# Kernel tuning notes

Measured on AMD Instinct MI355X. Metric: run time of the kernel, lower is better.

The kernel has to match this reference:

```python
import jax, jax.numpy as jnp
import numpy as np

E, QE, P, H = 3, 60000, 40, 20   # elements, atoms per element, fp length, hidden
NIMG = 1800                       # images in batch
Q = E * QE                        # total atoms
NNZ = 14_400_000                  # nnz of sparse fprimes [P*Q, 3*Q]


def setup_inputs() -> dict:
    key = jax.random.key(0)
    ks = jax.random.split(key, 12)
    fps = jax.random.normal(ks[0], (E, QE, P), jnp.float32)
    image_idx = jax.random.randint(ks[1], (E, QE), 0, NIMG, jnp.int32)
    s1 = 1.0 / np.sqrt(P)
    s2 = 1.0 / np.sqrt(H)
    W1 = (jax.random.normal(ks[2], (E, P, H)) * s1).astype(jnp.float32)
    b1 = jnp.zeros((E, H), jnp.float32)
    W2 = (jax.random.normal(ks[3], (E, H, H)) * s2).astype(jnp.float32)
    b2 = jnp.zeros((E, H), jnp.float32)
    W3 = (jax.random.normal(ks[4], (E, H, 1)) * s2).astype(jnp.float32)
    b3 = jnp.zeros((E, 1), jnp.float32)
    fp_rows = jax.random.randint(ks[5], (NNZ,), 0, P * Q, jnp.int32)
    fp_cols = jax.random.randint(ks[6], (NNZ,), 0, 3 * Q, jnp.int32)
    fp_vals = (jax.random.normal(ks[7], (NNZ,)) * 0.05).astype(jnp.float32)
    return {"fps": fps, "W1": W1, "b1": b1, "W2": W2, "b2": b2, "W3": W3,
            "b3": b3, "image_idx": image_idx, "fp_rows": fp_rows,
            "fp_cols": fp_cols, "fp_vals": fp_vals, "batch_size": NIMG}


def _mlp(x, w1, b1, w2, b2, w3, b3):
    # Dense(tanh) -> Dense(tanh) -> Dense(linear), per amptorch MLP(n_layers=3)
    h = jnp.tanh(x @ w1 + b1)
    h = jnp.tanh(h @ w2 + b2)
    return h @ w3 + b3  # [..., 1]


def _esum(x, w1, b1, w2, b2, w3, b3):
    return _mlp(x, w1, b1, w2, b2, w3, b3).sum()


def reference(fps, W1, b1, W2, b2, W3, b3, image_idx, fp_rows, fp_cols,
              fp_vals, batch_size):
    # per-element atomwise energies: [E, QE, 1]
    atom_e = jax.vmap(_mlp)(fps, W1, b1, W2, b2, W3, b3)
    # scatter-add atomic energies into per-image energies (index_add_)
    energy_pred = jax.ops.segment_sum(
        atom_e.reshape(-1, 1), image_idx.reshape(-1).astype(jnp.int32),
        num_segments=batch_size)  # [NIMG, 1]
    # dE/dFP per atom (each atom's output depends only on its own fp, so
    # grad of the per-element energy sum == per-atom jacobian rows)
    dE_dFP = jax.vmap(jax.grad(_esum))(fps, W1, b1, W2, b2, W3, b3)  # [E,QE,P]
    # reorder atoms from element-grouped order to image-index order
    # (stable argsort == boolean-match reorder in the torch code)
    order = jnp.argsort(image_idx.reshape(-1))
    dE_flat = dE_dFP.reshape(-1, P)[order].reshape(-1)  # [P*Q]
    # force = -fprimes^T @ dE_dFP  (sparse COO matvec via segment_sum)
    force_flat = -jax.ops.segment_sum(
        fp_vals * dE_flat[fp_rows], fp_cols, num_segments=3 * Q)
    force_pred = force_flat.reshape(-1, 3)  # [Q, 3]
    return energy_pred, force_pred
```

## Files before the change

kernel.cpp:

```cpp
#include <hip/hip_runtime.h>
#include <math.h>

#define E_    3
#define QE_   60000
#define QTOT  180000
#define P_    40
#define H_    20
#define NIMG_ 1800
#define NNZ_  14400000
#define BLK   256
#define NB    704

#define CW_BITS 12
#define CW      4096
#define NBIN    132
#define SUBS    8
#define SC      8192
#define NSB     1758
#define CAPB    114688

#define C_SCUR  0
#define C_BCUR  64
#define C_INTS  256

typedef int   vi4 __attribute__((ext_vector_type(4)));
typedef float vf4 __attribute__((ext_vector_type(4)));
typedef unsigned uint32;

__global__ void zero_kernel(float* __restrict__ out, int n) {
    int i = blockIdx.x * blockDim.x + threadIdx.x;
    if (i < n) out[i] = 0.0f;
}
__global__ void zero_ctrl_kernel(int* __restrict__ ctrl) {
    ctrl[threadIdx.x] = 0;
}

__global__ void hist_kernel(const int* __restrict__ img, int* __restrict__ g_hist) {
    __shared__ int h[NIMG_];
    const int t = threadIdx.x, b = blockIdx.x;
    for (int v = t; v < NIMG_; v += BLK) h[v] = 0;
    __syncthreads();
    int a = b * BLK + t;
    if (a < QTOT) atomicAdd(&h[img[a]], 1);
    __syncthreads();
    for (int v = t; v < NIMG_; v += BLK) g_hist[v * NB + b] = h[v];
}

__global__ void scan_blocks_kernel(int* __restrict__ g_hist, int* __restrict__ g_total) {
    __shared__ int s[BLK];
    const int v = blockIdx.x, t = threadIdx.x;
    int carry = 0;
    for (int c = 0; c < NB; c += BLK) {
        int idx = c + t;
        int val = (idx < NB) ? g_hist[v * NB + idx] : 0;
        s[t] = val; __syncthreads();
        for (int off = 1; off < BLK; off <<= 1) {
            int tmp = (t >= off) ? s[t - off] : 0;
            __syncthreads();
            s[t] += tmp;
            __syncthreads();
        }
        int excl = s[t] - val;
        int tot  = s[BLK - 1];
        if (idx < NB) g_hist[v * NB + idx] = carry + excl;
        carry += tot;
        __syncthreads();
    }
    if (t == 0) g_total[v] = carry;
}

__global__ void scan_buckets_kernel(const int* __restrict__ g_total, int* __restrict__ g_base) {
    __shared__ int s[BLK];
    const int t = threadIdx.x;
    int carry = 0;
    for (int c = 0; c < NIMG_; c += BLK) {
        int idx = c + t;
        int val = (idx < NIMG_) ? g_total[idx] : 0;
        s[t] = val; __syncthreads();
        for (int off = 1; off < BLK; off <<= 1) {
            int tmp = (t >= off) ? s[t - off] : 0;
            __syncthreads();
            s[t] += tmp;
            __syncthreads();
        }
        if (idx < NIMG_) g_base[idx] = carry + (s[t] - val);
        carry += s[BLK - 1];
        __syncthreads();
    }
}

__global__ void rank_kernel(const int* __restrict__ img, const int* __restrict__ g_hist,
                            const int* __restrict__ g_base, int* __restrict__ rank) {
    __shared__ int simg[BLK];
    const int t = threadIdx.x, b = blockIdx.x;
    int a = b * BLK + t;
    int v = (a < QTOT) ? img[a] : -1;
    simg[t] = v;
    __syncthreads();
    if (a < QTOT) {
        int local = 0;
        for (int j = 0; j < t; ++j) {
            if (simg[j] == v) local++;
        }
        rank[a] = g_base[v] + g_hist[v * NB + b] + local;
    }
}

__global__ __launch_bounds__(BLK) void mlp_kernel(
    const float* __restrict__ fps, const float* __restrict__ W1, const float* __restrict__ b1,
    const float* __restrict__ W2, const float* __restrict__ b2, const float* __restrict__ W3,
    const float* __restrict__ b3, const int* __restrict__ img, const int* __restrict__ rank,
    float* __restrict__ energy, float* __restrict__ dEflat)
{
    __shared__ float sW1[P_ * H_], sW2[H_ * H_], sW3[H_], sB1[H_], sB2[H_];
    __shared__ float sB3;
    const int e = blockIdx.y;
    const int t = threadIdx.x;
    for (int i = t; i < P_ * H_; i += BLK) sW1[i] = W1[e * P_ * H_ + i];
    for (int i = t; i < H_ * H_; i += BLK) sW2[i] = W2[e * H_ * H_ + i];
    if (t < H_) { sW3[t] = W3[e * H_ + t]; sB1[t] = b1[e * H_ + t]; sB2[t] = b2[e * H_ + t]; }
    if (t == 0) sB3 = b3[e];
    __syncthreads();

    int q = blockIdx.x * BLK + t;
    if (q >= QE_) return;
    int a = e * QE_ + q;

    const vf4* xp = (const vf4*)(fps + (size_t)a * P_);
    float x[P_];
    #pragma unroll
    for (int p = 0; p < P_; p += 4) {
        vf4 v4 = __builtin_nontemporal_load(xp + (p >> 2));
        x[p] = v4.x; x[p+1] = v4.y; x[p+2] = v4.z; x[p+3] = v4.w;
    }

    float h1v[H_], h2v[H_];
    #pragma unroll
    for (int i = 0; i < H_; ++i) {
        float z = sB1[i];
        #pragma unroll
        for (int p = 0; p < P_; ++p) z += x[p] * sW1[p * H_ + i];
        h1v[i] = tanhf(z);
    }
    #pragma unroll
    for (int i = 0; i < H_; ++i) {
        float z = sB2[i];
        #pragma unroll
        for (int j = 0; j < H_; ++j) z += h1v[j] * sW2[j * H_ + i];
        h2v[i] = tanhf(z);
    }
    float ea = sB3;
    #pragma unroll
    for (int i = 0; i < H_; ++i) ea += h2v[i] * sW3[i];
    atomicAdd(&energy[img[a]], ea);

    float dz2[H_];
    #pragma unroll
    for (int i = 0; i < H_; ++i) dz2[i] = sW3[i] * (1.0f - h2v[i] * h2v[i]);
    float dz1[H_];
    #pragma unroll
    for (int i = 0; i < H_; ++i) {
        float d = 0.0f;
        #pragma unroll
        for (int j = 0; j < H_; ++j) d += sW2[i * H_ + j] * dz2[j];
        dz1[i] = d * (1.0f - h1v[i] * h1v[i]);
    }
    float* op = dEflat + (size_t)rank[a] * P_;
    #pragma unroll
    for (int p = 0; p < P_; p += 4) {
        float4 v4;
        float d0 = 0.f, d1 = 0.f, d2 = 0.f, d3 = 0.f;
        #pragma unroll
        for (int i = 0; i < H_; ++i) {
            d0 += sW1[(p    ) * H_ + i] * dz1[i];
            d1 += sW1[(p + 1) * H_ + i] * dz1[i];
            d2 += sW1[(p + 2) * H_ + i] * dz1[i];
            d3 += sW1[(p + 3) * H_ + i] * dz1[i];
        }
        v4.x = d0; v4.y = d1; v4.z = d2; v4.w = d3;
        *(float4*)(op + p) = v4;
    }
}

__global__ __launch_bounds__(BLK) void binscatter_kernel(
    const int* __restrict__ rows, const int* __restrict__ cols, const float* __restrict__ vals,
    const float* __restrict__ dEflat, int* __restrict__ ctrl, uint32* __restrict__ bm)
{
    __shared__ uint32 itl[SC];
    __shared__ unsigned char bns[SC];
    __shared__ int hist[NBIN];
    __shared__ int cursor[NBIN];
    __shared__ int delta[NBIN];
    __shared__ int s[BLK];
    const int t = threadIdx.x, b = blockIdx.x;
    const int base = b * SC;
    const int nIt = min(SC, NNZ_ - base);
    const bool full = (nIt == SC);

    if (t < NBIN) hist[t] = 0;
    __syncthreads();
    if (full) {
        const vi4* c4 = (const vi4*)(cols + base);
        #pragma unroll
        for (int j = 0; j < SC / (BLK * 4); ++j) {
            vi4 cc = __builtin_nontemporal_load(c4 + j * BLK + t);
            atomicAdd(&hist[cc.x >> CW_BITS], 1);
            atomicAdd(&hist[cc.y >> CW_BITS], 1);
            atomicAdd(&hist[cc.z >> CW_BITS], 1);
            atomicAdd(&hist[cc.w >> CW_BITS], 1);
        }
    } else {
        for (int j = t; j < nIt; j += BLK)
            atomicAdd(&hist[cols[base + j] >> CW_BITS], 1);
    }
    __syncthreads();
    {
        int v = (t < NBIN) ? hist[t] : 0;
        s[t] = v; __syncthreads();
        for (int off = 1; off < BLK; off <<= 1) {
            int tmp = (t >= off) ? s[t - off] : 0;
            __syncthreads();
            s[t] += tmp;
            __syncthreads();
        }
        if (t < NBIN) {
            int ls = s[t] - v;
            cursor[t] = ls;
            int gb = (v > 0) ? atomicAdd(&ctrl[C_BCUR + t], v) : 0;
            delta[t] = t * CAPB + gb - ls;
        }
    }
    __syncthreads();
    #define PLACE(CI, VI, DI)                                                  \
    {                                                                          \
        int bin = (CI) >> CW_BITS;                                             \
        uint32 u = __float_as_uint(-(VI) * (DI));                              \
        uint32 pk = ((uint32)((CI) & (CW - 1)) << 20)                          \
                    | ((u + 0x800u) >> 12);                                    \
        int pos = atomicAdd(&cursor[bin], 1);                                  \
        itl[pos] = pk;                                                         \
        bns[pos] = (unsigned char)bin;                                         \
    }
    if (full) {
        const vi4* c4 = (const vi4*)(cols + base);
        const vi4* r4 = (const vi4*)(rows + base);
        const vf4* v4 = (const vf4*)(vals + base);
        #pragma unroll 2
        for (int j = 0; j < SC / (BLK * 4); ++j) {
            int idx = j * BLK + t;
            vi4 cc = __builtin_nontemporal_load(c4 + idx);
            vi4 rr = __builtin_nontemporal_load(r4 + idx);
            vf4 vv = __builtin_nontemporal_load(v4 + idx);
            float d0 = dEflat[rr.x];
            float d1 = dEflat[rr.y];
            float d2 = dEflat[rr.z];
            float d3 = dEflat[rr.w];
            PLACE(cc.x, vv.x, d0)
            PLACE(cc.y, vv.y, d1)
            PLACE(cc.z, vv.z, d2)
            PLACE(cc.w, vv.w, d3)
        }
    } else {
        for (int j = t; j < nIt; j += BLK) {
            int c = cols[base + j];
            float d = dEflat[rows[base + j]];
            float v = vals[base + j];
            PLACE(c, v, d)
        }
    }
    __syncthreads();
    for (int i = t; i < nIt; i += BLK) {
        __builtin_nontemporal_store(itl[i], &bm[delta[bns[i]] + i]);
    }
}

__global__ __launch_bounds__(BLK) void fforce4_kernel(
    const uint32* __restrict__ bm, const int* __restrict__ ctrl,
    float* __restrict__ partial)
{
    __shared__ float w[CW];
    const int t = threadIdx.x;
    const int bin = blockIdx.x >> 3;
    const int sub = blockIdx.x & (SUBS - 1);
    for (int i = t; i < CW; i += BLK) w[i] = 0.0f;
    __syncthreads();
    const int cnt   = ctrl[C_BCUR + bin];
    const int start = bin * CAPB;
    const int sBeg  = start + (cnt * sub) / SUBS;
    const int sEnd  = start + (cnt * (sub + 1)) / SUBS;
    int i = sBeg + t;
    for (; i + 3 * BLK < sEnd; i += 4 * BLK) {
        uint32 p0 = __builtin_nontemporal_load(bm + i);
        uint32 p1 = __builtin_nontemporal_load(bm + i + BLK);
        uint32 p2 = __builtin_nontemporal_load(bm + i + 2 * BLK);
        uint32 p3 = __builtin_nontemporal_load(bm + i + 3 * BLK);
        atomicAdd(&w[p0 >> 20], __uint_as_float((p0 & 0xFFFFFu) << 12));
        atomicAdd(&w[p1 >> 20], __uint_as_float((p1 & 0xFFFFFu) << 12));
        atomicAdd(&w[p2 >> 20], __uint_as_float((p2 & 0xFFFFFu) << 12));
        atomicAdd(&w[p3 >> 20], __uint_as_float((p3 & 0xFFFFFu) << 12));
    }
    for (; i < sEnd; i += BLK) {
        uint32 p = bm[i];
        atomicAdd(&w[p >> 20], __uint_as_float((p & 0xFFFFFu) << 12));
    }
    __syncthreads();
    float* dst = partial + (size_t)blockIdx.x * CW;
    for (int k = t; k < CW; k += BLK) __builtin_nontemporal_store(w[k], dst + k);
}

__global__ void freduce_kernel(const float* __restrict__ partial, float* __restrict__ force) {
    int i = blockIdx.x * BLK + threadIdx.x;
    if (i < 3 * QTOT) {
        int bin = i >> CW_BITS, local = i & (CW - 1);
        const float* p = partial + (size_t)bin * (CW * SUBS) + local;
        float sum = 0.0f;
        #pragma unroll
        for (int k = 0; k < SUBS; ++k) sum += __builtin_nontemporal_load(p + k * CW);
        force[i] = sum;
    }
}

__global__ void force_kernel(const int* __restrict__ rows, const int* __restrict__ cols,
                             const float* __restrict__ vals, const float* __restrict__ dEflat,
                             float* __restrict__ force) {
    int k = blockIdx.x * blockDim.x + threadIdx.x;
    if (k < NNZ_) {
        float contrib = -vals[k] * dEflat[rows[k]];
        atomicAdd(&force[cols[k]], contrib);
    }
}

extern "C" void kernel_launch(void* const* d_in, const int* in_sizes, int n_in,
                              void* d_out, int out_size, void* d_ws, size_t ws_size,
                              hipStream_t stream) {
    (void)in_sizes; (void)n_in; (void)out_size;
    const float* fps  = (const float*)d_in[0];
    const float* W1   = (const float*)d_in[1];
    const float* b1   = (const float*)d_in[2];
    const float* W2   = (const float*)d_in[3];
    const float* b2   = (const float*)d_in[4];
    const float* W3   = (const float*)d_in[5];
    const float* b3   = (const float*)d_in[6];
    const int*   img  = (const int*)d_in[7];
    const int*   rows = (const int*)d_in[8];
    const int*   cols = (const int*)d_in[9];
    const float* vals = (const float*)d_in[10];

    char* ws = (char*)d_ws;
    float* energy = (float*)d_out;
    float* force  = (float*)d_out + NIMG_;
    const int nOut = NIMG_ + 3 * QTOT;

    int*    g_hist  = (int*)(ws);
    int*    g_total = (int*)(ws + 5068800);
    int*    g_base  = (int*)(ws + 5076000);
    int*    rank    = (int*)(ws + 5083200);
    float*  partial4= (float*)(ws);
    uint32* bm4     = (uint32*)(ws + 118947840);
    int*    ctrl    = (int*)(ws + 179503104);
    float*  dEflat4 = (float*)(ws + 179536384);
    const size_t WS_V4 = 208336384;

    float*  dEflat5 = (float*)(ws + 5803200);
    const size_t WS_MIN = 5803200 + (size_t)QTOT * P_ * 4;

    const bool v4 = (ws_size >= WS_V4);
    float* dEflat = v4 ? dEflat4 : dEflat5;

    zero_kernel<<<(nOut + BLK - 1) / BLK, BLK, 0, stream>>>((float*)d_out, nOut);

    hist_kernel<<<NB, BLK, 0, stream>>>(img, g_hist);
    scan_blocks_kernel<<<NIMG_, BLK, 0, stream>>>(g_hist, g_total);
    scan_buckets_kernel<<<1, BLK, 0, stream>>>(g_total, g_base);
    rank_kernel<<<NB, BLK, 0, stream>>>(img, g_hist, g_base, rank);

    dim3 gm((QE_ + BLK - 1) / BLK, E_);
    mlp_kernel<<<gm, BLK, 0, stream>>>(fps, W1, b1, W2, b2, W3, b3, img, rank,
                                       energy, dEflat);

    if (v4) {
        zero_ctrl_kernel<<<1, 256, 0, stream>>>(ctrl);
        binscatter_kernel<<<NSB, BLK, 0, stream>>>(rows, cols, vals, dEflat, ctrl, bm4);
        fforce4_kernel<<<NBIN * SUBS, BLK, 0, stream>>>(bm4, ctrl, partial4);
        freduce_kernel<<<(3 * QTOT + BLK - 1) / BLK, BLK, 0, stream>>>(partial4, force);
    } else if (ws_size >= WS_MIN) {
        force_kernel<<<NNZ_ / BLK, BLK, 0, stream>>>(rows, cols, vals, dEflat, force);
    }
}
```

Measured before the change: 629.6 us.

## Pre-sort sparse entries by row slice so dE gathers hit cache

The force path now first partitions the nnz entries by row slice (128K rows each), with values truncated to 15 bits and packed alongside the row offset. A planning kernel then orders the chunks so that blocks in the same group share a row slice. The scatter pass gathers dEflat from a localized slice that should stay cache-resident, followed by a per-chunk column-bin histogram and scan so the column-binned output is compact. This replaces random gathers over the full 28.8 MB dEflat, but it adds an extra pass over 14.4M 8-byte items, several small launches, single-thread planning, and lower value precision.

```diff
diff --git a/kernel.cpp b/kernel.cpp
--- a/kernel.cpp
+++ b/kernel.cpp
@@ -17,11 +17,24 @@
 #define SUBS    8
 #define SC      8192
 #define NSB     1758
-#define CAPB    114688
+
+#define SLICE_SHIFT 17
+#define NSLICE  55
+
+#define GSPLIT  4
+#define NREG    220
+#define CAPS4   68096
+#define NCH4    2048
+#define NGMAX   384
+#define FS_GRID 1792
+#define FS_PERX 224
 
 #define C_SCUR  0
-#define C_BCUR  64
-#define C_INTS  256
+#define C_GCNT  256
+#define C_NCH   264
+#define C_CHID  512
+#define C_GRP   2560
+#define C_INTS  5632
 
 typedef int   vi4 __attribute__((ext_vector_type(4)));
 typedef float vf4 __attribute__((ext_vector_type(4)));
@@ -182,100 +195,250 @@
     }
 }
 
-__global__ __launch_bounds__(BLK) void binscatter_kernel(
+__global__ __launch_bounds__(BLK) void slice_scatter_kernel(
     const int* __restrict__ rows, const int* __restrict__ cols, const float* __restrict__ vals,
-    const float* __restrict__ dEflat, int* __restrict__ ctrl, uint32* __restrict__ bm)
+    int* __restrict__ ctrl, uint2* __restrict__ items)
 {
-    __shared__ uint32 itl[SC];
-    __shared__ unsigned char bns[SC];
-    __shared__ int hist[NBIN];
-    __shared__ int cursor[NBIN];
-    __shared__ int delta[NBIN];
-    __shared__ int s[BLK];
+    __shared__ uint32 srow[SC];
+    __shared__ int h[NSLICE], lcur[NSLICE], gbase[NSLICE];
     const int t = threadIdx.x, b = blockIdx.x;
+    const int g = b & (GSPLIT - 1);
     const int base = b * SC;
-    const int nIt = min(SC, NNZ_ - base);
-    const bool full = (nIt == SC);
-
-    if (t < NBIN) hist[t] = 0;
+    const int len = min(SC, NNZ_ - base);
+    const bool full = (len == SC);
+
+    if (t < NSLICE) h[t] = 0;
+    __syncthreads();
+    if (full) {
+        const vi4* r4 = (const vi4*)(rows + base);
+        #pragma unroll
+        for (int j = 0; j < SC / (BLK * 4); ++j) {
+            int idx = j * BLK + t;
+            vi4 rr = __builtin_nontemporal_load(r4 + idx);
+            srow[idx * 4 + 0] = (uint32)rr.x; atomicAdd(&h[rr.x >> SLICE_SHIFT], 1);
+            srow[idx * 4 + 1] = (uint32)rr.y; atomicAdd(&h[rr.y >> SLICE_SHIFT], 1);
+            srow[idx * 4 + 2] = (uint32)rr.z; atomicAdd(&h[rr.z >> SLICE_SHIFT], 1);
+            srow[idx * 4 + 3] = (uint32)rr.w; atomicAdd(&h[rr.w >> SLICE_SHIFT], 1);
+        }
+    } else {
+        for (int j = t; j < len; j += BLK) {
+            int r = rows[base + j];
+            srow[j] = (uint32)r;
+            atomicAdd(&h[r >> SLICE_SHIFT], 1);
+        }
+    }
+    __syncthreads();
+    if (t < NSLICE) {
+        lcur[t] = 0;
+        gbase[t] = (h[t] > 0) ? atomicAdd(&ctrl[C_SCUR + g * NSLICE + t], h[t]) : 0;
+    }
     __syncthreads();
     if (full) {
         const vi4* c4 = (const vi4*)(cols + base);
-        #pragma unroll
+        const vi4* v4 = (const vi4*)(vals + base);
+        #pragma unroll 2
         for (int j = 0; j < SC / (BLK * 4); ++j) {
-            vi4 cc = __builtin_nontemporal_load(c4 + j * BLK + t);
-            atomicAdd(&hist[cc.x >> CW_BITS], 1);
-            atomicAdd(&hist[cc.y >> CW_BITS], 1);
-            atomicAdd(&hist[cc.z >> CW_BITS], 1);
-            atomicAdd(&hist[cc.w >> CW_BITS], 1);
+            int idx = j * BLK + t;
+            vi4 cc = __builtin_nontemporal_load(c4 + idx);
+            vi4 vv = __builtin_nontemporal_load(v4 + idx);
+            #define EMIT(K, CI, VB)                                                \
+            {                                                                      \
+                uint32 r = srow[idx * 4 + K];                                      \
+                int sl = (int)(r >> SLICE_SHIFT);                                  \
+                int pos = gbase[sl] + atomicAdd(&lcur[sl], 1);                     \
+                uint32 v15 = (((uint32)(VB)) + 0x10000u) >> 17;                    \
+                items[(size_t)(g * NSLICE + sl) * CAPS4 + pos] =                   \
+                    make_uint2((v15 << 17) | (r & 0x1FFFFu), (uint32)(CI));        \
+            }
+            EMIT(0, cc.x, vv.x)
+            EMIT(1, cc.y, vv.y)
+            EMIT(2, cc.z, vv.z)
+            EMIT(3, cc.w, vv.w)
         }
     } else {
-        for (int j = t; j < nIt; j += BLK)
-            atomicAdd(&hist[cols[base + j] >> CW_BITS], 1);
-    }
-    __syncthreads();
-    {
-        int v = (t < NBIN) ? hist[t] : 0;
-        s[t] = v; __syncthreads();
+        for (int j = t; j < len; j += BLK) {
+            uint32 r = srow[j];
+            int sl = (int)(r >> SLICE_SHIFT);
+            int pos = gbase[sl] + atomicAdd(&lcur[sl], 1);
+            uint32 vb = ((const uint32*)vals)[base + j];
+            uint32 v15 = (vb + 0x10000u) >> 17;
+            items[(size_t)(g * NSLICE + sl) * CAPS4 + pos] =
+                make_uint2((v15 << 17) | (r & 0x1FFFFu), (uint32)cols[base + j]);
+        }
+    }
+}
+
+__global__ void plan4_kernel(int* __restrict__ ctrl) {
+    if (threadIdx.x == 0) {
+        int gp[8]; for (int i = 0; i < 8; ++i) gp[i] = 0;
+        int run = 0;
+        for (int gi = 0; gi < NREG; ++gi) {
+            int cnt = ctrl[C_SCUR + gi];
+            int nc = (cnt + SC - 1) / SC;
+            int x = (gi % NSLICE) & 7;
+            for (int c = 0; c < nc; ++c) {
+                ctrl[C_CHID + run] = (gi << 8) | c;
+                ctrl[C_GRP + x * NGMAX + gp[x]] = run;
+                gp[x]++; run++;
+            }
+        }
+        for (int i = 0; i < 8; ++i) ctrl[C_GCNT + i] = gp[i];
+        ctrl[C_NCH] = run;
+    }
+}
+
+__global__ __launch_bounds__(BLK) void fhist4_kernel(
+    const uint2* __restrict__ items, const int* __restrict__ ctrl,
+    int* __restrict__ binHist, unsigned short* __restrict__ binCnt)
+{
+    __shared__ int h[NBIN];
+    const int t = threadIdx.x, j = blockIdx.x;
+    const int tot = ctrl[C_NCH];
+    if (t < NBIN) h[t] = 0;
+    __syncthreads();
+    if (j < tot) {
+        const int pkd = ctrl[C_CHID + j];
+        const int gi = pkd >> 8, c = pkd & 255;
+        const int start = gi * CAPS4 + c * SC;
+        const int len = min(SC, ctrl[C_SCUR + gi] - c * SC);
+        if (len == SC) {
+            const vi4* p4 = (const vi4*)(items + start);
+            #pragma unroll
+            for (int k = 0; k < SC / (BLK * 2); ++k) {
+                vi4 q = __builtin_nontemporal_load(p4 + k * BLK + t);
+                atomicAdd(&h[((uint32)q.y) >> CW_BITS], 1);
+                atomicAdd(&h[((uint32)q.w) >> CW_BITS], 1);
+            }
+        } else {
+            for (int k = t; k < len; k += BLK)
+                atomicAdd(&h[items[start + k].y >> CW_BITS], 1);
+        }
+    }
+    __syncthreads();
+    if (t < NBIN) {
+        binHist[t * NCH4 + j] = h[t];
+        binCnt[t * NCH4 + j] = (unsigned short)h[t];
+    }
+}
+
+__global__ void fscan_blocks_kernel(int* __restrict__ binHist, int* __restrict__ binTotal,
+                                    int n) {
+    __shared__ int s[BLK];
+    const int v = blockIdx.x, t = threadIdx.x;
+    int carry = 0;
+    for (int c = 0; c < n; c += BLK) {
+        int idx = c + t;
+        int val = (idx < n) ? binHist[v * n + idx] : 0;
+        s[t] = val; __syncthreads();
         for (int off = 1; off < BLK; off <<= 1) {
             int tmp = (t >= off) ? s[t - off] : 0;
             __syncthreads();
             s[t] += tmp;
             __syncthreads();
         }
-        if (t < NBIN) {
-            int ls = s[t] - v;
-            cursor[t] = ls;
-            int gb = (v > 0) ? atomicAdd(&ctrl[C_BCUR + t], v) : 0;
-            delta[t] = t * CAPB + gb - ls;
-        }
-    }
-    __syncthreads();
-    #define PLACE(CI, VI, DI)                                                  \
-    {                                                                          \
-        int bin = (CI) >> CW_BITS;                                             \
-        uint32 u = __float_as_uint(-(VI) * (DI));                              \
-        uint32 pk = ((uint32)((CI) & (CW - 1)) << 20)                          \
-                    | ((u + 0x800u) >> 12);                                    \
-        int pos = atomicAdd(&cursor[bin], 1);                                  \
-        itl[pos] = pk;                                                         \
-        bns[pos] = (unsigned char)bin;                                         \
-    }
-    if (full) {
-        const vi4* c4 = (const vi4*)(cols + base);
-        const vi4* r4 = (const vi4*)(rows + base);
-        const vf4* v4 = (const vf4*)(vals + base);
-        #pragma unroll 2
-        for (int j = 0; j < SC / (BLK * 4); ++j) {
-            int idx = j * BLK + t;
-            vi4 cc = __builtin_nontemporal_load(c4 + idx);
-            vi4 rr = __builtin_nontemporal_load(r4 + idx);
-            vf4 vv = __builtin_nontemporal_load(v4 + idx);
-            float d0 = dEflat[rr.x];
-            float d1 = dEflat[rr.y];
-            float d2 = dEflat[rr.z];
-            float d3 = dEflat[rr.w];
-            PLACE(cc.x, vv.x, d0)
-            PLACE(cc.y, vv.y, d1)
-            PLACE(cc.z, vv.z, d2)
-            PLACE(cc.w, vv.w, d3)
-        }
-    } else {
-        for (int j = t; j < nIt; j += BLK) {
-            int c = cols[base + j];
-            float d = dEflat[rows[base + j]];
-            float v = vals[base + j];
-            PLACE(c, v, d)
-        }
-    }
-    __syncthreads();
-    for (int i = t; i < nIt; i += BLK) {
-        __builtin_nontemporal_store(itl[i], &bm[delta[bns[i]] + i]);
-    }
-}
-
-__global__ __launch_bounds__(BLK) void fforce4_kernel(
-    const uint32* __restrict__ bm, const int* __restrict__ ctrl,
+        int excl = s[t] - val;
+        int tot  = s[BLK - 1];
+        if (idx < n) binHist[v * n + idx] = carry + excl;
+        carry += tot;
+        __syncthreads();
+    }
+    if (t == 0) binTotal[v] = carry;
+}
+
+__global__ void fbase_kernel(const int* __restrict__ binTotal, int* __restrict__ binBase) {
+    __shared__ int s[BLK];
+    const int t = threadIdx.x;
+    int v = (t < NBIN) ? binTotal[t] : 0;
+    s[t] = v; __syncthreads();
+    for (int off = 1; off < BLK; off <<= 1) {
+        int tmp = (t >= off) ? s[t - off] : 0;
+        __syncthreads();
+        s[t] += tmp;
+        __syncthreads();
+    }
+    if (t < NBIN) binBase[t] = s[t] - v;
+    if (t == 0) binBase[NBIN] = s[BLK - 1];
+}
+
+__global__ __launch_bounds__(BLK) void fscatter4_kernel(
+    const uint2* __restrict__ items, const float* __restrict__ dEflat,
+    const int* __restrict__ ctrl, const int* __restrict__ binHist,
+    const unsigned short* __restrict__ binCnt, const int* __restrict__ binBase,
+    uint32* __restrict__ bm)
+{
+    __shared__ uint32 itl[SC];
+    __shared__ unsigned char bns[SC];
+    __shared__ int cur[NBIN], dlt[NBIN];
+    __shared__ int sc[BLK];
+    const int t = threadIdx.x;
+    const int x = blockIdx.x & 7;
+    const int r = blockIdx.x >> 3;
+    const int gc = ctrl[C_GCNT + x];
+
+    for (int w = r; w < gc; w += FS_PERX) {
+        const int j     = ctrl[C_GRP + x * NGMAX + w];
+        const int pkd   = ctrl[C_CHID + j];
+        const int gi    = pkd >> 8;
+        const int c     = pkd & 255;
+        const int start = gi * CAPS4 + c * SC;
+        const int len   = min(SC, ctrl[C_SCUR + gi] - c * SC);
+        const int sl    = gi % NSLICE;
+        const float* __restrict__ dE = dEflat + ((size_t)sl << SLICE_SHIFT);
+
+        {
+            int v = (t < NBIN) ? (int)binCnt[t * NCH4 + j] : 0;
+            sc[t] = v; __syncthreads();
+            for (int off = 1; off < BLK; off <<= 1) {
+                int tmp = (t >= off) ? sc[t - off] : 0;
+                __syncthreads();
+                sc[t] += tmp;
+                __syncthreads();
+            }
+            if (t < NBIN) {
+                int st = sc[t] - v;
+                cur[t] = st;
+                dlt[t] = binBase[t] + binHist[t * NCH4 + j] - st;
+            }
+        }
+        __syncthreads();
+        #define PLACE4(LO, CO, DI)                                             \
+        {                                                                      \
+            uint32 col = (uint32)(CO);                                         \
+            int bin = (int)(col >> CW_BITS);                                   \
+            float val = __uint_as_float((((uint32)(LO)) >> 17) << 17);         \
+            uint32 u = __float_as_uint(-val * (DI));                           \
+            uint32 pk = ((col & (CW - 1)) << 20) | ((u + 0x800u) >> 12);       \
+            int pos = atomicAdd(&cur[bin], 1);                                 \
+            itl[pos] = pk;                                                     \
+            bns[pos] = (unsigned char)bin;                                     \
+        }
+        if (len == SC) {
+            const vi4* p4 = (const vi4*)(items + start);
+            #pragma unroll 4
+            for (int k = 0; k < SC / (BLK * 2); ++k) {
+                vi4 q = __builtin_nontemporal_load(p4 + k * BLK + t);
+                float dA = dE[((uint32)q.x) & 0x1FFFFu];
+                float dB = dE[((uint32)q.z) & 0x1FFFFu];
+                PLACE4(q.x, q.y, dA)
+                PLACE4(q.z, q.w, dB)
+            }
+        } else {
+            for (int k = t; k < len; k += BLK) {
+                uint2 it = items[start + k];
+                float d = dE[it.x & 0x1FFFFu];
+                PLACE4(it.x, it.y, d)
+            }
+        }
+        __syncthreads();
+        for (int i = t; i < len; i += BLK) {
+            __builtin_nontemporal_store(itl[i], &bm[dlt[bns[i]] + i]);
+        }
+        __syncthreads();
+    }
+}
+
+__global__ __launch_bounds__(BLK) void fforce_kernel(
+    const uint32* __restrict__ bm, const int* __restrict__ binBase,
     float* __restrict__ partial)
 {
     __shared__ float w[CW];
@@ -284,8 +447,8 @@
     const int sub = blockIdx.x & (SUBS - 1);
     for (int i = t; i < CW; i += BLK) w[i] = 0.0f;
     __syncthreads();
-    const int cnt   = ctrl[C_BCUR + bin];
-    const int start = bin * CAPB;
+    const int start = binBase[bin];
+    const int cnt   = binBase[bin + 1] - start;
     const int sBeg  = start + (cnt * sub) / SUBS;
     const int sEnd  = start + (cnt * (sub + 1)) / SUBS;
     int i = sBeg + t;
@@ -351,14 +514,19 @@
     float* force  = (float*)d_out + NIMG_;
     const int nOut = NIMG_ + 3 * QTOT;
 
-    int*    g_hist  = (int*)(ws);
-    int*    g_total = (int*)(ws + 5068800);
-    int*    g_base  = (int*)(ws + 5076000);
-    int*    rank    = (int*)(ws + 5083200);
-    float*  partial4= (float*)(ws);
-    uint32* bm4     = (uint32*)(ws + 118947840);
-    int*    ctrl    = (int*)(ws + 179503104);
-    float*  dEflat4 = (float*)(ws + 179536384);
+    int*    g_hist   = (int*)(ws);
+    int*    g_total  = (int*)(ws + 5068800);
+    int*    g_base   = (int*)(ws + 5076000);
+    int*    rank     = (int*)(ws + 5083200);
+    uint2*  items    = (uint2*)(ws);
+    float*  partial4 = (float*)(ws);
+    uint32* bm4      = (uint32*)(ws + 119848960);
+    int*    binHist  = (int*)(ws + 177448960);
+    unsigned short* binCnt = (unsigned short*)(ws + 178530304);
+    int*    binTotal = (int*)(ws + 179070976);
+    int*    binBase  = (int*)(ws + 179071504);
+    int*    ctrl     = (int*)(ws + 179072064);
+    float*  dEflat4  = (float*)(ws + 179536384);
     const size_t WS_V4 = 208336384;
 
     float*  dEflat5 = (float*)(ws + 5803200);
@@ -379,9 +547,15 @@
                                        energy, dEflat);
 
     if (v4) {
-        zero_ctrl_kernel<<<1, 256, 0, stream>>>(ctrl);
-        binscatter_kernel<<<NSB, BLK, 0, stream>>>(rows, cols, vals, dEflat, ctrl, bm4);
-        fforce4_kernel<<<NBIN * SUBS, BLK, 0, stream>>>(bm4, ctrl, partial4);
+        zero_ctrl_kernel<<<1, 512, 0, stream>>>(ctrl);
+        slice_scatter_kernel<<<NSB, BLK, 0, stream>>>(rows, cols, vals, ctrl, items);
+        plan4_kernel<<<1, BLK, 0, stream>>>(ctrl);
+        fhist4_kernel<<<NCH4, BLK, 0, stream>>>(items, ctrl, binHist, binCnt);
+        fscan_blocks_kernel<<<NBIN, BLK, 0, stream>>>(binHist, binTotal, NCH4);
+        fbase_kernel<<<1, BLK, 0, stream>>>(binTotal, binBase);
+        fscatter4_kernel<<<FS_GRID, BLK, 0, stream>>>(items, dEflat, ctrl,
+                                                      binHist, binCnt, binBase, bm4);
+        fforce_kernel<<<NBIN * SUBS, BLK, 0, stream>>>(bm4, binBase, partial4);
         freduce_kernel<<<(3 * QTOT + BLK - 1) / BLK, BLK, 0, stream>>>(partial4, force);
     } else if (ws_size >= WS_MIN) {
         force_kernel<<<NNZ_ / BLK, BLK, 0, stream>>>(rows, cols, vals, dEflat, force);
```

Result: slower. 802.8 us (+27.5%).
